# Kernel tuning notes

Measured on AMD Instinct MI355X. Metric: run time of the kernel, lower is better.

## Reference

```python
import jax, jax.numpy as jnp
import numpy as np

N_NODES = 100000
N_EDGES = 1600000
IN_DIM, HID_DIM, OUT_DIM = 128, 128, 64


def setup_inputs() -> dict:
    key = jax.random.key(0)
    ks = jax.random.split(key, 5)
    x = jax.random.normal(ks[0], (N_NODES, IN_DIM), dtype=jnp.float32)
    edge_index = jax.random.randint(ks[1], (2, N_EDGES), 0, N_NODES, dtype=jnp.int64)
    W1 = jax.random.normal(ks[2], (IN_DIM, HID_DIM), dtype=jnp.float32) * (1.0 / np.sqrt(IN_DIM))
    b1 = jnp.zeros((HID_DIM,), dtype=jnp.float32)
    W2 = jax.random.normal(ks[3], (HID_DIM, OUT_DIM), dtype=jnp.float32) * (1.0 / np.sqrt(HID_DIM))
    b2 = jnp.zeros((OUT_DIM,), dtype=jnp.float32)
    return {"x": x, "edge_index": edge_index, "W1": W1, "b1": b1, "W2": W2, "b2": b2}


def _gcn_conv(h, row, col, norm, b, n_nodes):
    # h: [N, F] already linearly transformed; message = norm_e * h[src]; scatter-add to dst
    msg = h[row] * norm[:, None]                      # [E+N, F]
    out = jax.ops.segment_sum(msg, col, num_segments=n_nodes)
    return out + b


def reference(x, edge_index, W1, b1, W2, b2):
    n = x.shape[0]
    loops = jnp.arange(n, dtype=edge_index.dtype)
    row = jnp.concatenate([edge_index[0], loops])     # sources (incl. self loops)
    col = jnp.concatenate([edge_index[1], loops])     # targets
    # symmetric normalization: deg over targets with unit edge weights
    deg = jax.ops.segment_sum(jnp.ones_like(col, dtype=x.dtype), col, num_segments=n)
    dinv = jnp.where(deg > 0, jax.lax.rsqrt(jnp.maximum(deg, 1.0)), 0.0)
    norm = dinv[row] * dinv[col]                      # [E+N]
    h = jax.nn.relu(_gcn_conv(x @ W1, row, col, norm, b1, n))
    out = _gcn_conv(h @ W2, row, col, norm, b2, n)
    return out.mean(axis=0)                           # [OUT_DIM]
```

## Files before the change

### kernel.cpp

```cpp
#include <hip/hip_runtime.h>

#define N_NODES 100000
#define N_EDGES 1600000
#define IN_DIM 128
#define HID_DIM 128
#define OUT_DIM 64
#define BKT_SHIFT 7
#define BKT_SIZE 128
#define NBKT ((N_NODES + BKT_SIZE - 1) / BKT_SIZE)
#define B1 256
#define HIST_N (NBKT * B1)
#define HIST_N2 (2 * HIST_N)
#define GEMM_BLKS ((N_NODES + 127) / 128)
#define AGG_BLKS 2048
#define NPW 13

typedef float v2f __attribute__((ext_vector_type(2)));
typedef float v4f __attribute__((ext_vector_type(4)));
typedef short v8s __attribute__((ext_vector_type(8)));

__device__ __forceinline__ int permb(int b) { return ((b & 7) << 5) | (b >> 3); }

__device__ __forceinline__ unsigned int f2bf(float f) {
  unsigned int u = __float_as_uint(f);
  return (u + 0x7FFFu + ((u >> 16) & 1u)) >> 16;
}

template <bool HI>
__device__ __forceinline__ v2f cvt8(unsigned int u) {
  return __builtin_amdgcn_cvt_pk_f32_fp8((int)u, HI);
}

__device__ __forceinline__ float redq(float v) {
  v += __shfl_xor(v, 16);
  v += __shfl_xor(v, 32);
  return v;
}

__device__ __forceinline__ void load4(const void* ei, int is64, int half, int base,
                                      int* v) {
  if (is64) {
    const long long* e = (const long long*)ei + (size_t)half * N_EDGES + base;
    longlong2 a = *(const longlong2*)e;
    longlong2 b = *(const longlong2*)(e + 2);
    v[0] = (int)a.x; v[1] = (int)a.y; v[2] = (int)b.x; v[3] = (int)b.y;
  } else {
    const int* e = (const int*)ei + (size_t)half * N_EDGES + base;
    int4 a = *(const int4*)e;
    v[0] = a.x; v[1] = a.y; v[2] = a.z; v[3] = a.w;
  }
}

__device__ __forceinline__ int detect64_block(const unsigned int* ei, int* sh) {
  if (threadIdx.x == 0) *sh = 0;
  __syncthreads();
  if (ei[1 + 2 * threadIdx.x] != 0u) *sh = 1;
  __syncthreads();
  return (*sh == 0) ? 1 : 0;
}

__global__ __launch_bounds__(256) void front_kernel(const float* __restrict__ x,
                                                    const float* __restrict__ W,
                                                    const void* ei,
                                                    unsigned int* __restrict__ G,
                                                    int* hist, float* S) {
  __shared__ __align__(16) char smem[128 * 136 * 2];
  if (blockIdx.x >= GEMM_BLKS) {
    int* hd = (int*)smem;
    int* hs = hd + NBKT;
    int* sh = hs + NBKT;
    const int hb = blockIdx.x - GEMM_BLKS;
    const int pj = permb(hb);
    if (hb == 0 && threadIdx.x < HID_DIM) S[threadIdx.x] = 0.f;
    const int is64 = detect64_block((const unsigned int*)ei, sh);
    for (int k = threadIdx.x; k < NBKT; k += 256) { hd[k] = 0; hs[k] = 0; }
    __syncthreads();
    for (int g = hb * 256 + threadIdx.x; g < N_EDGES / 4; g += B1 * 256) {
      int r[4], c[4];
      load4(ei, is64, 0, g * 4, r);
      load4(ei, is64, 1, g * 4, c);
#pragma unroll
      for (int k = 0; k < 4; k++) {
        atomicAdd(&hd[c[k] >> BKT_SHIFT], 1);
        atomicAdd(&hs[r[k] >> BKT_SHIFT], 1);
      }
    }
    __syncthreads();
    for (int k = threadIdx.x; k < NBKT; k += 256) {
      hist[k * B1 + pj] = hd[k];
      hist[HIST_N + k * B1 + pj] = hs[k];
    }
    return;
  }
  typedef unsigned short us_row[136];
  us_row* lwt = (us_row*)smem;
  const int t = threadIdx.x;
  const int row0 = blockIdx.x * 128;

  const int lane = t & 63;
  const int wv = t >> 6;
  const int m0 = wv * 32;
  const int lrow = lane & 15;
  const int lk = (lane >> 4) * 8;

  v8s a0r[4], a1r[4];
  {
    const int r0 = row0 + m0 + lrow;
    const int r1 = r0 + 16;
    const float* x0 = x + (size_t)r0 * IN_DIM + lk;
    const float* x1 = x + (size_t)r1 * IN_DIM + lk;
    const bool ok0 = r0 < N_NODES, ok1 = r1 < N_NODES;
    const float4 z4 = make_float4(0.f, 0.f, 0.f, 0.f);
#pragma unroll
    for (int kq = 0; kq < 4; ++kq) {
      float4 fa = z4, fb = z4, fc = z4, fd = z4;
      if (ok0) { fa = *(const float4*)(x0 + kq * 32); fb = *(const float4*)(x0 + kq * 32 + 4); }
      if (ok1) { fc = *(const float4*)(x1 + kq * 32); fd = *(const float4*)(x1 + kq * 32 + 4); }
      v8s p, q;
      p[0] = (short)f2bf(fa.x); p[1] = (short)f2bf(fa.y);
      p[2] = (short)f2bf(fa.z); p[3] = (short)f2bf(fa.w);
      p[4] = (short)f2bf(fb.x); p[5] = (short)f2bf(fb.y);
      p[6] = (short)f2bf(fb.z); p[7] = (short)f2bf(fb.w);
      q[0] = (short)f2bf(fc.x); q[1] = (short)f2bf(fc.y);
      q[2] = (short)f2bf(fc.z); q[3] = (short)f2bf(fc.w);
      q[4] = (short)f2bf(fd.x); q[5] = (short)f2bf(fd.y);
      q[6] = (short)f2bf(fd.z); q[7] = (short)f2bf(fd.w);
      a0r[kq] = p;
      a1r[kq] = q;
    }
  }

  {
    const float4* W4 = (const float4*)W;
    for (int it = 0; it < 16; ++it) {
      int idx = t + 256 * it;
      int k = idx >> 5, c4 = (idx & 31) * 4;
      float4 w = W4[idx];
      lwt[c4 + 0][k] = (unsigned short)f2bf(w.x);
      lwt[c4 + 1][k] = (unsigned short)f2bf(w.y);
      lwt[c4 + 2][k] = (unsigned short)f2bf(w.z);
      lwt[c4 + 3][k] = (unsigned short)f2bf(w.w);
    }
  }
  __syncthreads();

  v4f acc[2][8];
#pragma unroll
  for (int si = 0; si < 2; si++)
#pragma unroll
    for (int n = 0; n < 8; n++) acc[si][n] = (v4f){0.f, 0.f, 0.f, 0.f};

#pragma unroll
  for (int kq = 0; kq < 4; ++kq) {
    const int kk = kq * 32;
    const v8s a0 = a0r[kq];
    const v8s a1 = a1r[kq];
#pragma unroll
    for (int n = 0; n < 8; n++) {
      v8s b = *(const v8s*)&lwt[n * 16 + lrow][kk + lk];
      acc[0][n] = __builtin_amdgcn_mfma_f32_16x16x32_bf16(a0, b, acc[0][n], 0, 0, 0);
      acc[1][n] = __builtin_amdgcn_mfma_f32_16x16x32_bf16(a1, b, acc[1][n], 0, 0, 0);
    }
  }

  uint2* Gv = (uint2*)G;
#pragma unroll
  for (int si = 0; si < 2; si++)
#pragma unroll
    for (int i = 0; i < 4; i++) {
      const int rr = row0 + m0 + si * 16 + (lane >> 4) * 4 + i;
      if (rr < N_NODES) {
        int w0 = __builtin_amdgcn_cvt_pk_fp8_f32(acc[si][0][i], acc[si][1][i], 0, false);
        w0 = __builtin_amdgcn_cvt_pk_fp8_f32(acc[si][2][i], acc[si][3][i], w0, true);
        int w1 = __builtin_amdgcn_cvt_pk_fp8_f32(acc[si][4][i], acc[si][5][i], 0, false);
        w1 = __builtin_amdgcn_cvt_pk_fp8_f32(acc[si][6][i], acc[si][7][i], w1, true);
        Gv[(size_t)rr * 16 + lrow] = make_uint2((unsigned)w0, (unsigned)w1);
      }
    }
}

__global__ void scan1_kernel(int* arr, int* bsum, int n) {
  __shared__ int tmp[256];
  int i = blockIdx.x * 256 + threadIdx.x;
  int v = (i < n) ? arr[i] : 0;
  tmp[threadIdx.x] = v;
  __syncthreads();
  for (int off = 1; off < 256; off <<= 1) {
    int t2 = (threadIdx.x >= off) ? tmp[threadIdx.x - off] : 0;
    __syncthreads();
    tmp[threadIdx.x] += t2;
    __syncthreads();
  }
  if (i < n) arr[i] = tmp[threadIdx.x] - v;
  if (threadIdx.x == 255) bsum[blockIdx.x] = tmp[255];
}

__global__ void scan2_kernel(int* bsum, int nb) {
  __shared__ int tmp[1024];
  const int t = threadIdx.x;
  int v0 = (2 * t < nb) ? bsum[2 * t] : 0;
  int v1 = (2 * t + 1 < nb) ? bsum[2 * t + 1] : 0;
  int s = v0 + v1;
  tmp[t] = s;
  __syncthreads();
  for (int off = 1; off < 1024; off <<= 1) {
    int t2 = (t >= off) ? tmp[t - off] : 0;
    __syncthreads();
    tmp[t] += t2;
    __syncthreads();
  }
  int excl = tmp[t] - s;
  if (2 * t < nb) bsum[2 * t] = excl;
  if (2 * t + 1 < nb) bsum[2 * t + 1] = excl + v0;
}

__global__ __launch_bounds__(256) void scatter_kernel(const void* ei, const int* hist,
                                                      const int* bsum,
                                                      unsigned int* pairs) {
  __shared__ int cd[NBKT], cs[NBKT], sh[1];
  const int is64 = detect64_block((const unsigned int*)ei, sh);
  const int pj = permb(blockIdx.x);
  for (int k = threadIdx.x; k < NBKT; k += 256) {
    cd[k] = hist[k * B1 + pj] + bsum[k];
    cs[k] = hist[HIST_N + k * B1 + pj] + bsum[NBKT + k];
  }
  __syncthreads();
  for (int g = blockIdx.x * 256 + threadIdx.x; g < N_EDGES / 4; g += B1 * 256) {
    int r[4], c[4];
    load4(ei, is64, 0, g * 4, r);
    load4(ei, is64, 1, g * 4, c);
#pragma unroll
    for (int k = 0; k < 4; k++) {
      int pd = atomicAdd(&cd[c[k] >> BKT_SHIFT], 1);
      pairs[pd] = ((unsigned int)(c[k] & (BKT_SIZE - 1)) << 17) | (unsigned int)r[k];
      int ps = atomicAdd(&cs[r[k] >> BKT_SHIFT], 1);
      pairs[ps] = ((unsigned int)(r[k] & (BKT_SIZE - 1)) << 17) | (unsigned int)c[k];
    }
  }
}

__global__ __launch_bounds__(256) void csrA_kernel(const int* hist, const int* bsum,
                                                   const unsigned int* pairs,
                                                   int* rowptr, float* dinv) {
  __shared__ int cnt[BKT_SIZE], sc[BKT_SIZE];
  const int k = blockIdx.x;
  const int base = hist[k * B1] + bsum[k];
  const int end = (k == NBKT - 1) ? N_EDGES : hist[(k + 1) * B1] + bsum[k + 1];
  const int nseg = end - base;
  const int l = threadIdx.x;
  if (l < BKT_SIZE) cnt[l] = 0;
  __syncthreads();
  for (int i = l; i < nseg; i += 256) atomicAdd(&cnt[pairs[base + i] >> 17], 1);
  __syncthreads();
  if (l < BKT_SIZE) sc[l] = cnt[l];
  __syncthreads();
  for (int off = 1; off < BKT_SIZE; off <<= 1) {
    int v = (l < BKT_SIZE && l >= off) ? sc[l - off] : 0;
    __syncthreads();
    if (l < BKT_SIZE) sc[l] += v;
    __syncthreads();
  }
  if (l < BKT_SIZE) {
    int excl = sc[l] - cnt[l];
    int v = k * BKT_SIZE + l;
    if (v < N_NODES) {
      rowptr[v] = base + excl;
      dinv[v] = rsqrtf((float)(cnt[l] + 1));
    }
  }
  if (k == NBKT - 1 && l == 0) rowptr[N_NODES] = N_EDGES;
}

__global__ __launch_bounds__(256) void csrBout_kernel(const int* hist, const int* bsum,
                                                      const unsigned int* pairs,
                                                      const int* __restrict__ rowptr,
                                                      const float* __restrict__ dinv,
                                                      unsigned int* __restrict__ csr,
                                                      float* __restrict__ wacc) {
  if (blockIdx.x < NBKT) {
    __shared__ int cur[BKT_SIZE];
    const int k = blockIdx.x;
    const int base = hist[k * B1] + bsum[k];
    const int end = (k == NBKT - 1) ? N_EDGES : hist[(k + 1) * B1] + bsum[k + 1];
    const int nseg = end - base;
    const int l = threadIdx.x;
    if (l < BKT_SIZE) {
      int v = k * BKT_SIZE + l;
      cur[l] = (v < N_NODES) ? rowptr[v] : 0;
    }
    __syncthreads();
    int i = l;
    for (; i + 768 < nseg; i += 1024) {
      const unsigned int pk0 = pairs[base + i];
      const unsigned int pk1 = pairs[base + i + 256];
      const unsigned int pk2 = pairs[base + i + 512];
      const unsigned int pk3 = pairs[base + i + 768];
      const unsigned int s0 = pk0 & 0x1FFFFu, s1 = pk1 & 0x1FFFFu;
      const unsigned int s2 = pk2 & 0x1FFFFu, s3 = pk3 & 0x1FFFFu;
      const float d0 = dinv[s0], d1 = dinv[s1], d2 = dinv[s2], d3 = dinv[s3];
      const int p0 = atomicAdd(&cur[pk0 >> 17], 1);
      const int p1 = atomicAdd(&cur[pk1 >> 17], 1);
      const int p2 = atomicAdd(&cur[pk2 >> 17], 1);
      const int p3 = atomicAdd(&cur[pk3 >> 17], 1);
      csr[p0] = (f2bf(d0) << 17) | s0;
      csr[p1] = (f2bf(d1) << 17) | s1;
      csr[p2] = (f2bf(d2) << 17) | s2;
      csr[p3] = (f2bf(d3) << 17) | s3;
    }
    for (; i < nseg; i += 256) {
      const unsigned int pk = pairs[base + i];
      const unsigned int src = pk & 0x1FFFFu;
      const int pos = atomicAdd(&cur[pk >> 17], 1);
      csr[pos] = (f2bf(dinv[src]) << 17) | src;
    }
    return;
  }
  __shared__ float fb[BKT_SIZE];
  const int k = blockIdx.x - NBKT;
  const int base = hist[HIST_N + k * B1] + bsum[NBKT + k];
  const int end =
      (k == NBKT - 1) ? 2 * N_EDGES : hist[HIST_N + (k + 1) * B1] + bsum[NBKT + k + 1];
  if (threadIdx.x < BKT_SIZE) fb[threadIdx.x] = 0.f;
  __syncthreads();
  int i = base + threadIdx.x;
  for (; i + 768 < end; i += 1024) {
    const unsigned int pk0 = pairs[i];
    const unsigned int pk1 = pairs[i + 256];
    const unsigned int pk2 = pairs[i + 512];
    const unsigned int pk3 = pairs[i + 768];
    const float d0 = dinv[pk0 & 0x1FFFFu];
    const float d1 = dinv[pk1 & 0x1FFFFu];
    const float d2 = dinv[pk2 & 0x1FFFFu];
    const float d3 = dinv[pk3 & 0x1FFFFu];
    atomicAdd(&fb[pk0 >> 17], d0);
    atomicAdd(&fb[pk1 >> 17], d1);
    atomicAdd(&fb[pk2 >> 17], d2);
    atomicAdd(&fb[pk3 >> 17], d3);
  }
  for (; i < end; i += 256) {
    const unsigned int pk = pairs[i];
    atomicAdd(&fb[pk >> 17], dinv[pk & 0x1FFFFu]);
  }
  __syncthreads();
  int v = k * BKT_SIZE + threadIdx.x;
  if (threadIdx.x < BKT_SIZE && v < N_NODES) wacc[v] = fb[threadIdx.x];
}

__global__ __launch_bounds__(256) void aggregate_kernel(
    const unsigned int* __restrict__ G, const int* __restrict__ rowptr,
    const unsigned int* __restrict__ csr, const float* __restrict__ dinv,
    const float* __restrict__ wacc, const float* __restrict__ b1,
    float* __restrict__ S) {
  __shared__ float lb[HID_DIM];
  __shared__ float ls[HID_DIM];
  if (threadIdx.x < HID_DIM) {
    lb[threadIdx.x] = b1[threadIdx.x];
    ls[threadIdx.x] = 0.f;
  }
  __syncthreads();

  const int lane = threadIdx.x & 63;
  const int q = lane >> 4;
  const int r = lane & 15;
  const int wid = blockIdx.x * 4 + (threadIdx.x >> 6);
  const int c0 = wid * NPW;
  const uint2* __restrict__ G2 = (const uint2*)G;

  int rp = 0;
  float dvv = 0.f, wvv = 0.f;
  {
    const int ci = c0 + lane;
    if (lane <= NPW && ci <= N_NODES) rp = rowptr[ci];
    if (lane < NPW && ci < N_NODES) { dvv = dinv[ci]; wvv = wacc[ci]; }
  }

  v2f s01 = {0.f, 0.f}, s23 = {0.f, 0.f}, s45 = {0.f, 0.f}, s67 = {0.f, 0.f};
  const int nn = (c0 < N_NODES) ? min(NPW, N_NODES - c0) : 0;

  if (nn > 0) {
    int kF = 0, jF = 0;
    const int sF0 = __shfl(rp, 0);
    int cnumF = __shfl(rp, 1) - sF0;
    int SF = max(1, (cnumF + 15) >> 4);
    unsigned int pwW = 0;
    if (lane < cnumF) pwW = __builtin_nontemporal_load(&csr[sF0 + lane]);
    int sN = __shfl(rp, 1);
    int eN = __shfl(rp, 2);
    unsigned int pwN = 0;
    if (1 < nn && sN + lane < eN) pwN = __builtin_nontemporal_load(&csr[sN + lane]);

    int kC = 0, jC = 0;
    int SC = SF;
    float dC = __shfl(dvv, 0), waC = __shfl(wvv, 0);
    v2f a01 = {0.f, 0.f}, a23 = {0.f, 0.f}, a45 = {0.f, 0.f}, a67 = {0.f, 0.f};

    uint2 gA[4], gB[4], gSA, gSB;
    unsigned int wpA[2], wpB[2];

    auto FETCH = [&](uint2(&g)[4], unsigned int(&wp)[2], uint2& gS) {
      if (jF != 0 && (jF & 3) == 0) {
        const int sAbs = __shfl(rp, kF) + (jF << 4);
        pwW = 0;
        if ((jF << 4) + lane < cnumF)
          pwW = __builtin_nontemporal_load(&csr[sAbs + lane]);
      }
      const int base = (jF & 3) << 4;
      const int eg0 = (jF << 4) + q;
      unsigned int wb[4];
#pragma unroll
      for (int t = 0; t < 4; ++t) {
        const unsigned int p = __shfl(pwW, base + 4 * t + q);
        const bool vld = eg0 + 4 * t < cnumF;
        wb[t] = vld ? ((p >> 17) << 16) : 0u;
        g[t] = make_uint2(0u, 0u);
        if (vld) g[t] = G2[(size_t)(p & 0x1FFFFu) * 16 + r];
      }
      wp[0] = wb[0] | (wb[1] >> 16);
      wp[1] = wb[2] | (wb[3] >> 16);
      if (jF == 0) {
        gS = make_uint2(0u, 0u);
        if (q == 0) gS = G2[(size_t)(c0 + kF) * 16 + r];
      }
      if (jF + 1 < SF) { jF++; return; }
      kF++; jF = 0;
      if (kF < nn) {
        pwW = pwN;
        cnumF = eN - sN;
        SF = max(1, (cnumF + 15) >> 4);
        if (kF + 1 < nn) {
          sN = __shfl(rp, kF + 1);
          eN = __shfl(rp, kF + 2);
          pwN = 0;
          if (sN + lane < eN) pwN = __builtin_nontemporal_load(&csr[sN + lane]);
        }
      }
    };

    auto CONSUME = [&](const uint2(&g)[4], const unsigned int(&wp)[2],
                       const uint2& gS) -> bool {
      const float w0 = __uint_as_float(wp[0] & 0xFFFF0000u);
      const float w1 = __uint_as_float(wp[0] << 16);
      const float w2 = __uint_as_float(wp[1] & 0xFFFF0000u);
      const float w3 = __uint_as_float(wp[1] << 16);
      a01 += cvt8<false>(g[0].x) * w0; a23 += cvt8<true>(g[0].x) * w0;
      a45 += cvt8<false>(g[0].y) * w0; a67 += cvt8<true>(g[0].y) * w0;
      a01 += cvt8<false>(g[1].x) * w1; a23 += cvt8<true>(g[1].x) * w1;
      a45 += cvt8<false>(g[1].y) * w1; a67 += cvt8<true>(g[1].y) * w1;
      a01 += cvt8<false>(g[2].x) * w2; a23 += cvt8<true>(g[2].x) * w2;
      a45 += cvt8<false>(g[2].y) * w2; a67 += cvt8<true>(g[2].y) * w2;
      a01 += cvt8<false>(g[3].x) * w3; a23 += cvt8<true>(g[3].x) * w3;
      a45 += cvt8<false>(g[3].y) * w3; a67 += cvt8<true>(g[3].y) * w3;
      if (jC == 0 && q == 0) {
        a01 += cvt8<false>(gS.x) * dC; a23 += cvt8<true>(gS.x) * dC;
        a45 += cvt8<false>(gS.y) * dC; a67 += cvt8<true>(gS.y) * dC;
      }
      if (jC + 1 < SC) { jC++; return true; }
      const float A0 = redq(a01.x), A1 = redq(a01.y);
      const float A2 = redq(a23.x), A3 = redq(a23.y);
      const float A4 = redq(a45.x), A5 = redq(a45.y);
      const float A6 = redq(a67.x), A7 = redq(a67.y);
      if (q == 0) {
        const float wc = dC * (waC + dC);
        s01.x += wc * fmaxf(fmaf(dC, A0, lb[r]), 0.f);
        s01.y += wc * fmaxf(fmaf(dC, A1, lb[r + 16]), 0.f);
        s23.x += wc * fmaxf(fmaf(dC, A2, lb[r + 32]), 0.f);
        s23.y += wc * fmaxf(fmaf(dC, A3, lb[r + 48]), 0.f);
        s45.x += wc * fmaxf(fmaf(dC, A4, lb[r + 64]), 0.f);
        s45.y += wc * fmaxf(fmaf(dC, A5, lb[r + 80]), 0.f);
        s67.x += wc * fmaxf(fmaf(dC, A6, lb[r + 96]), 0.f);
        s67.y += wc * fmaxf(fmaf(dC, A7, lb[r + 112]), 0.f);
      }
      a01 = (v2f){0.f, 0.f}; a23 = (v2f){0.f, 0.f};
      a45 = (v2f){0.f, 0.f}; a67 = (v2f){0.f, 0.f};
      kC++; jC = 0;
      if (kC >= nn) return false;
      const int s_ = __shfl(rp, kC);
      const int cnumC = __shfl(rp, kC + 1) - s_;
      SC = max(1, (cnumC + 15) >> 4);
      dC = __shfl(dvv, kC);
      waC = __shfl(wvv, kC);
      return true;
    };

    FETCH(gA, wpA, gSA);
    for (;;) {
      if (kF < nn) FETCH(gB, wpB, gSB);
      if (!CONSUME(gA, wpA, gSA)) break;
      if (kF < nn) FETCH(gA, wpA, gSA);
      if (!CONSUME(gB, wpB, gSB)) break;
    }
  }

  if (q == 0) {
    atomicAdd(&ls[r], s01.x);       atomicAdd(&ls[r + 16], s01.y);
    atomicAdd(&ls[r + 32], s23.x);  atomicAdd(&ls[r + 48], s23.y);
    atomicAdd(&ls[r + 64], s45.x);  atomicAdd(&ls[r + 80], s45.y);
    atomicAdd(&ls[r + 96], s67.x);  atomicAdd(&ls[r + 112], s67.y);
  }
  __syncthreads();
  if (threadIdx.x < HID_DIM) atomicAdd(&S[threadIdx.x], ls[threadIdx.x]);
}

__global__ void finish_kernel(const float* __restrict__ S, const float* __restrict__ W2,
                              const float* __restrict__ b2, float* __restrict__ out) {
  int j = threadIdx.x;
  float acc = 0.f;
  for (int k = 0; k < HID_DIM; k++) acc += S[k] * W2[k * OUT_DIM + j];
  out[j] = acc * (1.0f / N_NODES) + b2[j];
}

extern "C" void kernel_launch(void* const* d_in, const int* in_sizes, int n_in,
                              void* d_out, int out_size, void* d_ws, size_t ws_size,
                              hipStream_t stream) {
  const float* x  = (const float*)d_in[0];
  const void*  ei = d_in[1];
  const float* W1 = (const float*)d_in[2];
  const float* b1 = (const float*)d_in[3];
  const float* W2 = (const float*)d_in[4];
  const float* b2 = (const float*)d_in[5];
  float* out = (float*)d_out;

  char* p = (char*)d_ws;
  size_t off = 0;
  auto alloc = [&](size_t bytes) -> void* {
    void* r = p + off;
    off = (off + bytes + 63) & ~(size_t)63;
    return r;
  };
  int*   hist   = (int*)alloc((size_t)HIST_N2 * 4);
  int*   bsum   = (int*)alloc(2048 * 4);
  unsigned int* pairs = (unsigned int*)alloc((size_t)2 * N_EDGES * 4);
  int*   rowptr = (int*)alloc(((size_t)N_NODES + 1) * 4);
  unsigned int* csr = (unsigned int*)alloc((size_t)N_EDGES * 4);
  float* dinv   = (float*)alloc((size_t)N_NODES * 4);
  float* wacc   = (float*)alloc((size_t)N_NODES * 4);
  float* S      = (float*)alloc(HID_DIM * 4);
  unsigned int* G = (unsigned int*)alloc((size_t)N_NODES * HID_DIM);
  (void)ws_size; (void)n_in; (void)in_sizes; (void)out_size;

  const int NBH = HIST_N2 / 256;

  front_kernel<<<GEMM_BLKS + B1, 256, 0, stream>>>(x, W1, ei, G, hist, S);
  scan1_kernel<<<NBH, 256, 0, stream>>>(hist, bsum, HIST_N2);
  scan2_kernel<<<1, 1024, 0, stream>>>(bsum, NBH);
  scatter_kernel<<<B1, 256, 0, stream>>>(ei, hist, bsum, pairs);
  csrA_kernel<<<NBKT, 256, 0, stream>>>(hist, bsum, pairs, rowptr, dinv);
  csrBout_kernel<<<2 * NBKT, 256, 0, stream>>>(hist, bsum, pairs, rowptr, dinv, csr,
                                               wacc);
  aggregate_kernel<<<AGG_BLKS, 256, 0, stream>>>(G, rowptr, csr, dinv, wacc, b1, S);
  finish_kernel<<<1, 64, 0, stream>>>(S, W2, b2, out);
}
```

Measured before the change: 258.1 us.

## Split GEMM across scatter and CSR kernels to overlap with graph preprocessing

Moves the X@W1 MFMA GEMM out of the front histogram kernel and spreads its row tiles over the scatter kernel (391 tiles) and the csrBout kernel (the remaining tiles), which run as extra blocks. The histogram becomes its own small kernel. The W tile in LDS is halved to 64 columns, loaded twice with a sync in between, so that shared memory fits the combined kernels. The aim is to hide the GEMM behind the latency-bound, atomic-heavy scatter and CSR phases and to shorten the critical path before those phases start. The cost is a second W load-and-convert pass with an extra barrier, and larger shared-memory footprints in the scatter and CSR kernels, which may reduce their occupancy.

```diff
diff --git a/kernel.cpp b/kernel.cpp
--- a/kernel.cpp
+++ b/kernel.cpp
@@ -12,6 +12,7 @@
 #define HIST_N (NBKT * B1)
 #define HIST_N2 (2 * HIST_N)
 #define GEMM_BLKS ((N_NODES + 127) / 128)
+#define GEMM_A 391
 #define AGG_BLKS 2048
 #define NPW 13
 
@@ -59,44 +60,11 @@
   return (*sh == 0) ? 1 : 0;
 }
 
-__global__ __launch_bounds__(256) void front_kernel(const float* __restrict__ x,
-                                                    const float* __restrict__ W,
-                                                    const void* ei,
-                                                    unsigned int* __restrict__ G,
-                                                    int* hist, float* S) {
-  __shared__ __align__(16) char smem[128 * 136 * 2];
-  if (blockIdx.x >= GEMM_BLKS) {
-    int* hd = (int*)smem;
-    int* hs = hd + NBKT;
-    int* sh = hs + NBKT;
-    const int hb = blockIdx.x - GEMM_BLKS;
-    const int pj = permb(hb);
-    if (hb == 0 && threadIdx.x < HID_DIM) S[threadIdx.x] = 0.f;
-    const int is64 = detect64_block((const unsigned int*)ei, sh);
-    for (int k = threadIdx.x; k < NBKT; k += 256) { hd[k] = 0; hs[k] = 0; }
-    __syncthreads();
-    for (int g = hb * 256 + threadIdx.x; g < N_EDGES / 4; g += B1 * 256) {
-      int r[4], c[4];
-      load4(ei, is64, 0, g * 4, r);
-      load4(ei, is64, 1, g * 4, c);
-#pragma unroll
-      for (int k = 0; k < 4; k++) {
-        atomicAdd(&hd[c[k] >> BKT_SHIFT], 1);
-        atomicAdd(&hs[r[k] >> BKT_SHIFT], 1);
-      }
-    }
-    __syncthreads();
-    for (int k = threadIdx.x; k < NBKT; k += 256) {
-      hist[k * B1 + pj] = hd[k];
-      hist[HIST_N + k * B1 + pj] = hs[k];
-    }
-    return;
-  }
+__device__ void gemm_role(const float* __restrict__ x, const float* __restrict__ W,
+                          unsigned int* __restrict__ G, int row0, char* smem) {
   typedef unsigned short us_row[136];
   us_row* lwt = (us_row*)smem;
   const int t = threadIdx.x;
-  const int row0 = blockIdx.x * 128;
-
   const int lane = t & 63;
   const int wv = t >> 6;
   const int m0 = wv * 32;
@@ -130,20 +98,6 @@
     }
   }
 
-  {
-    const float4* W4 = (const float4*)W;
-    for (int it = 0; it < 16; ++it) {
-      int idx = t + 256 * it;
-      int k = idx >> 5, c4 = (idx & 31) * 4;
-      float4 w = W4[idx];
-      lwt[c4 + 0][k] = (unsigned short)f2bf(w.x);
-      lwt[c4 + 1][k] = (unsigned short)f2bf(w.y);
-      lwt[c4 + 2][k] = (unsigned short)f2bf(w.z);
-      lwt[c4 + 3][k] = (unsigned short)f2bf(w.w);
-    }
-  }
-  __syncthreads();
-
   v4f acc[2][8];
 #pragma unroll
   for (int si = 0; si < 2; si++)
@@ -151,15 +105,34 @@
     for (int n = 0; n < 8; n++) acc[si][n] = (v4f){0.f, 0.f, 0.f, 0.f};
 
 #pragma unroll
-  for (int kq = 0; kq < 4; ++kq) {
-    const int kk = kq * 32;
-    const v8s a0 = a0r[kq];
-    const v8s a1 = a1r[kq];
-#pragma unroll
-    for (int n = 0; n < 8; n++) {
-      v8s b = *(const v8s*)&lwt[n * 16 + lrow][kk + lk];
-      acc[0][n] = __builtin_amdgcn_mfma_f32_16x16x32_bf16(a0, b, acc[0][n], 0, 0, 0);
-      acc[1][n] = __builtin_amdgcn_mfma_f32_16x16x32_bf16(a1, b, acc[1][n], 0, 0, 0);
+  for (int h = 0; h < 2; ++h) {
+    if (h) __syncthreads();
+    {
+      const float4* W4 = (const float4*)W;
+#pragma unroll
+      for (int it = 0; it < 8; ++it) {
+        const int idx = t + 256 * it;
+        const int k = idx >> 4, c4 = (idx & 15) * 4;
+        float4 w = W4[k * 32 + 16 * h + (idx & 15)];
+        lwt[c4 + 0][k] = (unsigned short)f2bf(w.x);
+        lwt[c4 + 1][k] = (unsigned short)f2bf(w.y);
+        lwt[c4 + 2][k] = (unsigned short)f2bf(w.z);
+        lwt[c4 + 3][k] = (unsigned short)f2bf(w.w);
+      }
+    }
+    __syncthreads();
+#pragma unroll
+    for (int kq = 0; kq < 4; ++kq) {
+      const int kk = kq * 32;
+      const v8s a0 = a0r[kq];
+      const v8s a1 = a1r[kq];
+#pragma unroll
+      for (int nl = 0; nl < 4; nl++) {
+        const int n = 4 * h + nl;
+        v8s b = *(const v8s*)&lwt[nl * 16 + lrow][kk + lk];
+        acc[0][n] = __builtin_amdgcn_mfma_f32_16x16x32_bf16(a0, b, acc[0][n], 0, 0, 0);
+        acc[1][n] = __builtin_amdgcn_mfma_f32_16x16x32_bf16(a1, b, acc[1][n], 0, 0, 0);
+      }
     }
   }
 
@@ -179,6 +152,32 @@
     }
 }
 
+__global__ __launch_bounds__(256) void hist_kernel(const void* ei, int* hist,
+                                                   float* S) {
+  __shared__ int hd[NBKT], hs[NBKT], sh[1];
+  const int hb = blockIdx.x;
+  const int pj = permb(hb);
+  if (hb == 0 && threadIdx.x < HID_DIM) S[threadIdx.x] = 0.f;
+  const int is64 = detect64_block((const unsigned int*)ei, sh);
+  for (int k = threadIdx.x; k < NBKT; k += 256) { hd[k] = 0; hs[k] = 0; }
+  __syncthreads();
+  for (int g = hb * 256 + threadIdx.x; g < N_EDGES / 4; g += B1 * 256) {
+    int r[4], c[4];
+    load4(ei, is64, 0, g * 4, r);
+    load4(ei, is64, 1, g * 4, c);
+#pragma unroll
+    for (int k = 0; k < 4; k++) {
+      atomicAdd(&hd[c[k] >> BKT_SHIFT], 1);
+      atomicAdd(&hs[r[k] >> BKT_SHIFT], 1);
+    }
+  }
+  __syncthreads();
+  for (int k = threadIdx.x; k < NBKT; k += 256) {
+    hist[k * B1 + pj] = hd[k];
+    hist[HIST_N + k * B1 + pj] = hs[k];
+  }
+}
+
 __global__ void scan1_kernel(int* arr, int* bsum, int n) {
   __shared__ int tmp[256];
   int i = blockIdx.x * 256 + threadIdx.x;
@@ -216,8 +215,18 @@
 
 __global__ __launch_bounds__(256) void scatter_kernel(const void* ei, const int* hist,
                                                       const int* bsum,
-                                                      unsigned int* pairs) {
-  __shared__ int cd[NBKT], cs[NBKT], sh[1];
+                                                      unsigned int* pairs,
+                                                      const float* __restrict__ x,
+                                                      const float* __restrict__ W,
+                                                      unsigned int* __restrict__ G) {
+  __shared__ __align__(16) char smem[64 * 136 * 2];
+  if (blockIdx.x >= B1) {
+    gemm_role(x, W, G, (blockIdx.x - B1) * 128, smem);
+    return;
+  }
+  int* cd = (int*)smem;
+  int* cs = cd + NBKT;
+  int* sh = cs + NBKT;
   const int is64 = detect64_block((const unsigned int*)ei, sh);
   const int pj = permb(blockIdx.x);
   for (int k = threadIdx.x; k < NBKT; k += 256) {
@@ -276,9 +285,17 @@
                                                       const int* __restrict__ rowptr,
                                                       const float* __restrict__ dinv,
                                                       unsigned int* __restrict__ csr,
-                                                      float* __restrict__ wacc) {
+                                                      float* __restrict__ wacc,
+                                                      const float* __restrict__ x,
+                                                      const float* __restrict__ W,
+                                                      unsigned int* __restrict__ G) {
+  __shared__ __align__(16) char smem[64 * 136 * 2];
+  if (blockIdx.x >= 2 * NBKT) {
+    gemm_role(x, W, G, (GEMM_A + blockIdx.x - 2 * NBKT) * 128, smem);
+    return;
+  }
   if (blockIdx.x < NBKT) {
-    __shared__ int cur[BKT_SIZE];
+    int* cur = (int*)smem;
     const int k = blockIdx.x;
     const int base = hist[k * B1] + bsum[k];
     const int end = (k == NBKT - 1) ? N_EDGES : hist[(k + 1) * B1] + bsum[k + 1];
@@ -315,7 +332,7 @@
     }
     return;
   }
-  __shared__ float fb[BKT_SIZE];
+  float* fb = (float*)smem;
   const int k = blockIdx.x - NBKT;
   const int base = hist[HIST_N + k * B1] + bsum[NBKT + k];
   const int end =
@@ -540,13 +557,13 @@
 
   const int NBH = HIST_N2 / 256;
 
-  front_kernel<<<GEMM_BLKS + B1, 256, 0, stream>>>(x, W1, ei, G, hist, S);
+  hist_kernel<<<B1, 256, 0, stream>>>(ei, hist, S);
   scan1_kernel<<<NBH, 256, 0, stream>>>(hist, bsum, HIST_N2);
   scan2_kernel<<<1, 1024, 0, stream>>>(bsum, NBH);
-  scatter_kernel<<<B1, 256, 0, stream>>>(ei, hist, bsum, pairs);
+  scatter_kernel<<<B1 + GEMM_A, 256, 0, stream>>>(ei, hist, bsum, pairs, x, W1, G);
   csrA_kernel<<<NBKT, 256, 0, stream>>>(hist, bsum, pairs, rowptr, dinv);
-  csrBout_kernel<<<2 * NBKT, 256, 0, stream>>>(hist, bsum, pairs, rowptr, dinv, csr,
-                                               wacc);
+  csrBout_kernel<<<2 * NBKT + (GEMM_BLKS - GEMM_A), 256, 0, stream>>>(
+      hist, bsum, pairs, rowptr, dinv, csr, wacc, x, W1, G);
   aggregate_kernel<<<AGG_BLKS, 256, 0, stream>>>(G, rowptr, csr, dinv, wacc, b1, S);
   finish_kernel<<<1, 64, 0, stream>>>(S, W2, b2, out);
 }
```

Result: slower. 277.3 us (+7.4%).
